# Optimization experiments

Measured on AMD Instinct MI355X. Metric: run time of the kernel, lower is better.

Reference implementation:

```python
import jax, jax.numpy as jnp
import numpy as np

N = 50000        # nodes
E = 800000       # edges (before self-loops)
F_IN = 128       # num_features
HID = 32         # hidden_size per head
HEADS = 4
CLS = 40         # num_classes
NEG_SLOPE = 0.2  # PyG GATConv default leaky_relu slope


def setup_inputs() -> dict:
    key = jax.random.key(0)
    ks = jax.random.split(key, 10)
    s = lambda k, sh: (jax.random.normal(k, sh, jnp.float32) * 0.05)
    x = jax.random.normal(ks[0], (N, F_IN), jnp.float32)
    edge_index = jax.random.randint(ks[1], (2, E), 0, N, dtype=jnp.int64)
    W1 = s(ks[2], (F_IN, HEADS * HID))
    att_src1 = s(ks[3], (HEADS, HID))
    att_dst1 = s(ks[4], (HEADS, HID))
    b1 = jnp.zeros((HEADS * HID,), jnp.float32)
    W2 = s(ks[5], (HEADS * HID, CLS))
    att_src2 = s(ks[6], (1, CLS))
    att_dst2 = s(ks[7], (1, CLS))
    b2 = jnp.zeros((CLS,), jnp.float32)
    return {"x": x, "edge_index": edge_index, "W1": W1, "att_src1": att_src1,
            "att_dst1": att_dst1, "b1": b1, "W2": W2, "att_src2": att_src2,
            "att_dst2": att_dst2, "b2": b2}


def _add_self_loops(edge_index, num_nodes):
    ar = jnp.arange(num_nodes, dtype=edge_index.dtype)
    loops = jnp.stack([ar, ar])
    return jnp.concatenate([edge_index, loops], axis=1)


def _gat_conv(x, edge_index, W, a_src, a_dst, bias, heads, concat):
    """PyG GATConv (eval mode, additive attention, self-loops already added)."""
    n = x.shape[0]
    src, dst = edge_index[0], edge_index[1]
    h = (x @ W).reshape(n, heads, -1)                 # [N, H, C]
    a_s = jnp.einsum('nhc,hc->nh', h, a_src)          # [N, H]
    a_d = jnp.einsum('nhc,hc->nh', h, a_dst)          # [N, H]
    e = jax.nn.leaky_relu(a_s[src] + a_d[dst], NEG_SLOPE)   # [E', H]
    m = jax.ops.segment_max(e, dst, num_segments=n)   # segment softmax over dst
    ex = jnp.exp(e - m[dst])
    den = jax.ops.segment_sum(ex, dst, num_segments=n)
    alpha = ex / den[dst]                             # [E', H]
    out = jax.ops.segment_sum(h[src] * alpha[:, :, None], dst, num_segments=n)
    out = out.reshape(n, -1) if concat else out.mean(axis=1)
    return out + bias


def reference(x, edge_index, W1, att_src1, att_dst1, b1, W2, att_src2, att_dst2, b2):
    ei = _add_self_loops(edge_index, x.shape[0])
    # dropout p=0 in eval -> identity
    h = jax.nn.relu(_gat_conv(x, ei, W1, att_src1, att_dst1, b1, HEADS, True))
    out = _gat_conv(h, ei, W2, att_src2, att_dst2, b2, 1, True)  # heads=1
    return out
```

## Files before the change

### kernel.cpp

```cpp
#include <hip/hip_runtime.h>
#include <cstdint>

#define NODES 50000
#define FIN   128
#define C1    128
#define HEADS 4
#define HID   32
#define CLS   40
#define SLOPE 0.2f

#define NBUCK ((NODES + 255) >> 8)
#define EPB 2048
#define BCAP 8192

__device__ __forceinline__ float lrelu(float v) { return v > 0.f ? v : SLOPE * v; }

__device__ __forceinline__ unsigned short f2bf(float f) {
    union { float f; unsigned u; } v; v.f = f;
    unsigned u = v.u;
    return (unsigned short)((u + 0x7FFFu + ((u >> 16) & 1u)) >> 16);
}
__device__ __forceinline__ float bf2f(unsigned short b) {
    union { unsigned u; float f; } v; v.u = ((unsigned)b) << 16;
    return v.f;
}
__device__ __forceinline__ float bflo(unsigned u) {
    union { unsigned x; float f; } v; v.x = u << 16; return v.f;
}
__device__ __forceinline__ float bfhi(unsigned u) {
    union { unsigned x; float f; } v; v.x = u & 0xffff0000u; return v.f;
}
__device__ __forceinline__ unsigned cvtpk(float a, float b) {
    unsigned r;
    asm("v_cvt_pk_bf16_f32 %0, %1, %2" : "=v"(r) : "v"(a), "v"(b));
    return r;
}

typedef __attribute__((ext_vector_type(8))) short bf16x8;
typedef __attribute__((ext_vector_type(4))) float f32x4;
typedef __attribute__((ext_vector_type(4), aligned(4))) int int4a;

__device__ __forceinline__ void acc8(float w, uint4 p, float* ac) {
    ac[0] = fmaf(w, bflo(p.x), ac[0]); ac[1] = fmaf(w, bfhi(p.x), ac[1]);
    ac[2] = fmaf(w, bflo(p.y), ac[2]); ac[3] = fmaf(w, bfhi(p.y), ac[3]);
    ac[4] = fmaf(w, bflo(p.z), ac[4]); ac[5] = fmaf(w, bfhi(p.z), ac[5]);
    ac[6] = fmaf(w, bflo(p.w), ac[6]); ac[7] = fmaf(w, bfhi(p.w), ac[7]);
}

__global__ __launch_bounds__(256) void k_prep(const float* __restrict__ W1,
                                              const float* __restrict__ W2,
                                              unsigned short* __restrict__ w1t,
                                              unsigned short* __restrict__ w2t,
                                              int* __restrict__ bwp) {
    const int b = blockIdx.x, t = threadIdx.x;
    if (b < 8) {
        __shared__ unsigned short Tb[16][136];
        const int n0 = b * 16;
        const int k = t & 127, g = t >> 7;
#pragma unroll
        for (int i = 0; i < 8; i++)
            Tb[g * 8 + i][k] = f2bf(W1[(size_t)k * C1 + n0 + g * 8 + i]);
        __syncthreads();
        {
            int nl = t >> 4, k8 = (t & 15) * 8;
            *(uint4*)(w1t + (n0 + nl) * 128 + k8) = *(uint4*)(&Tb[nl][k8]);
        }
    } else {
        for (int p = t; p < CLS * 128; p += 256) {
            int n = p >> 7, k = p & 127;
            w2t[n * 128 + k] = f2bf(W2[(size_t)k * CLS + n]);
        }
        if (t < NBUCK) bwp[t] = t * BCAP;
    }
}

__global__ __launch_bounds__(256) void k_front(const float* __restrict__ X,
                                               const unsigned short* __restrict__ w1t,
                                               const float* __restrict__ AS,
                                               const float* __restrict__ AD,
                                               unsigned short* __restrict__ h1b,
                                               float* __restrict__ as1,
                                               float* __restrict__ ad1,
                                               const int* __restrict__ src,
                                               const int* __restrict__ dst, int E,
                                               int* __restrict__ bwp,
                                               int* __restrict__ tmp, int GB1) {
    __shared__ unsigned short Asm[64][136];
    __shared__ unsigned short Wt[128][136];
    __shared__ int cnt[NBUCK];
    __shared__ int bbs[NBUCK];
    const int t = threadIdx.x;

    if (blockIdx.x >= GB1) {
        for (int i = t; i < NBUCK; i += 256) cnt[i] = 0;
        __syncthreads();
        const int e0 = (blockIdx.x - GB1) * EPB;
        int v[8], rb[8];
#pragma unroll
        for (int k = 0; k < 8; k++) {
            int e = e0 + k * 256 + t;
            rb[k] = -1;
            if (e < E) {
                int d = dst[e], s = src[e];
                int b = d >> 8;
                int r = atomicAdd(&cnt[b], 1);
                v[k] = (s << 8) | (d & 255);
                rb[k] = (r << 8) | b;
            }
        }
        __syncthreads();
        for (int i = t; i < NBUCK; i += 256) {
            int c = cnt[i];
            bbs[i] = c ? atomicAdd(&bwp[i], c) : 0;
        }
        __syncthreads();
#pragma unroll
        for (int k = 0; k < 8; k++) {
            if (rb[k] >= 0) {
                int b = rb[k] & 255;
                int r = rb[k] >> 8;
                tmp[bbs[b] + r] = v[k];
            }
        }
        return;
    }

    const int row0 = blockIdx.x * 64;
#pragma unroll
    for (int i = 0; i < 8; i++) {
        int p = i * 256 + t;
        int n = p >> 4, k8 = (p & 15) * 8;
        *(uint4*)(&Wt[n][k8]) = *(const uint4*)(w1t + n * 128 + k8);
    }
    {
        int r = t >> 2, c0 = (t & 3) * 32;
        int gr = row0 + r;
        if (gr < NODES) {
#pragma unroll
            for (int i = 0; i < 4; i++) {
                float4 va = *(const float4*)(X + (size_t)gr * FIN + c0 + i * 8);
                float4 vb = *(const float4*)(X + (size_t)gr * FIN + c0 + i * 8 + 4);
                uint4 pk;
                pk.x = cvtpk(va.x, va.y);
                pk.y = cvtpk(va.z, va.w);
                pk.z = cvtpk(vb.x, vb.y);
                pk.w = cvtpk(vb.z, vb.w);
                *(uint4*)(&Asm[r][c0 + i * 8]) = pk;
            }
        } else {
            uint4 z = make_uint4(0, 0, 0, 0);
#pragma unroll
            for (int i = 0; i < 4; i++) *(uint4*)(&Asm[r][c0 + i * 8]) = z;
        }
    }
    __syncthreads();

    const int w = t >> 6, l = t & 63;
    const int lm = l & 15, quad = l >> 4;
    f32x4 acc[8];
#pragma unroll
    for (int ct = 0; ct < 8; ct++) acc[ct] = (f32x4){0.f, 0.f, 0.f, 0.f};
#pragma unroll
    for (int kt = 0; kt < 4; kt++) {
        bf16x8 a = *(const bf16x8*)(&Asm[w * 16 + lm][kt * 32 + quad * 8]);
#pragma unroll
        for (int ct = 0; ct < 8; ct++) {
            bf16x8 b = *(const bf16x8*)(&Wt[ct * 16 + lm][kt * 32 + quad * 8]);
            acc[ct] = __builtin_amdgcn_mfma_f32_16x16x32_bf16(a, b, acc[ct], 0, 0, 0);
        }
    }
    __syncthreads();
#pragma unroll
    for (int ct = 0; ct < 8; ct++)
#pragma unroll
        for (int r = 0; r < 4; r++)
            Asm[w * 16 + quad * 4 + r][ct * 16 + lm] = f2bf(acc[ct][r]);
    __syncthreads();
    {
        int r = t >> 2, c0 = (t & 3) * 32;
        int gr = row0 + r;
        if (gr < NODES) {
#pragma unroll
            for (int i = 0; i < 4; i++)
                *(uint4*)(h1b + (size_t)gr * C1 + c0 + i * 8) =
                    *(uint4*)(&Asm[r][c0 + i * 8]);
        }
    }
    {
        int r = t >> 2, h = t & 3;
        int gr = row0 + r;
        if (gr < NODES) {
            float s = 0.f, d = 0.f;
#pragma unroll
            for (int j = 0; j < 32; j++) {
                float v = bf2f(Asm[r][h * 32 + j]);
                s = fmaf(v, AS[h * HID + j], s);
                d = fmaf(v, AD[h * HID + j], d);
            }
            as1[gr * HEADS + h] = s;
            ad1[gr * HEADS + h] = d;
        }
    }
}

__global__ __launch_bounds__(256) void k_bucketB(const int* __restrict__ bwp,
                                                 const int* __restrict__ tmp,
                                                 int* __restrict__ col,
                                                 int* __restrict__ rowptr,
                                                 int* __restrict__ degarr) {
    __shared__ int degs[256];
    __shared__ int wp[256];
    __shared__ int wsum[4];
    const int b = blockIdx.x, t = threadIdx.x;
    const int n0 = b << 8;
    const int beg = b * BCAP;
    const int end = bwp[b];
    degs[t] = 0;
    __syncthreads();
    for (int e = beg + t; e < end; e += 256)
        atomicAdd(&degs[tmp[e] & 255], 1);
    __syncthreads();
    const int d = degs[t];
    int incl = d;
    const int lane = t & 63, w = t >> 6;
#pragma unroll
    for (int s = 1; s < 64; s <<= 1) {
        int u = __shfl_up(incl, s);
        if (lane >= s) incl += u;
    }
    if (lane == 63) wsum[w] = incl;
    __syncthreads();
    if (t == 0) {
        int r = 0;
#pragma unroll
        for (int i = 0; i < 4; i++) { int x = wsum[i]; wsum[i] = r; r += x; }
    }
    __syncthreads();
    const int excl = incl - d + wsum[w] + beg;
    const int nidx = n0 + t;
    if (nidx < NODES) { rowptr[nidx] = excl; degarr[nidx] = d; }
    wp[t] = excl;
    __syncthreads();
    for (int e = beg + t; e < end; e += 256) {
        int v = tmp[e];
        int p = atomicAdd(&wp[v & 255], 1);
        col[p] = v >> 8;
    }
}

__global__ __launch_bounds__(256) void k_agg1(const unsigned short* __restrict__ h1b,
                                              const float* __restrict__ as1,
                                              const float* __restrict__ ad1,
                                              const int* __restrict__ rowptr,
                                              const int* __restrict__ degarr,
                                              const int* __restrict__ col,
                                              const float* __restrict__ b1,
                                              unsigned short* __restrict__ out1) {
    int wid = (blockIdx.x * 256 + threadIdx.x) >> 6;
    if (wid >= NODES) return;
    const int lane = threadIdx.x & 63;
    const int q  = lane >> 4;
    const int ll = lane & 15;
    const int fh = ll >> 2;
    const int n = wid;
    const float adn = ad1[n * HEADS + fh];
    const int rs = rowptr[n];
    const int re = rs + degarr[n];

    float den = 0.f;
    float ac[8];
#pragma unroll
    for (int k = 0; k < 8; k++) ac[k] = 0.f;

    for (int base = rs; base < re; base += 32) {
        int4a ca = *(const int4a*)(col + base + q * 4);
        int4a cb = *(const int4a*)(col + base + 16 + q * 4);
        const int ia = base + q * 4;
        const int ib = base + 16 + q * 4;
        int c0 = (ia + 0 < re) ? ca.x : n;
        int c1 = (ia + 1 < re) ? ca.y : n;
        int c2 = (ia + 2 < re) ? ca.z : n;
        int c3 = (ia + 3 < re) ? ca.w : n;
        int c4 = (ib + 0 < re) ? cb.x : n;
        int c5 = (ib + 1 < re) ? cb.y : n;
        int c6 = (ib + 2 < re) ? cb.z : n;
        int c7 = (ib + 3 < re) ? cb.w : n;
        float w0 = __expf(lrelu(as1[c0 * HEADS + fh] + adn)); if (ia + 0 >= re) w0 = 0.f;
        float w1 = __expf(lrelu(as1[c1 * HEADS + fh] + adn)); if (ia + 1 >= re) w1 = 0.f;
        float w2 = __expf(lrelu(as1[c2 * HEADS + fh] + adn)); if (ia + 2 >= re) w2 = 0.f;
        float w3 = __expf(lrelu(as1[c3 * HEADS + fh] + adn)); if (ia + 3 >= re) w3 = 0.f;
        float w4 = __expf(lrelu(as1[c4 * HEADS + fh] + adn)); if (ib + 0 >= re) w4 = 0.f;
        float w5 = __expf(lrelu(as1[c5 * HEADS + fh] + adn)); if (ib + 1 >= re) w5 = 0.f;
        float w6 = __expf(lrelu(as1[c6 * HEADS + fh] + adn)); if (ib + 2 >= re) w6 = 0.f;
        float w7 = __expf(lrelu(as1[c7 * HEADS + fh] + adn)); if (ib + 3 >= re) w7 = 0.f;
        den += ((w0 + w1) + (w2 + w3)) + ((w4 + w5) + (w6 + w7));
        const unsigned lo = (unsigned)(ll << 4);
        uint4 p0 = *(const uint4*)((const char*)h1b + (((unsigned)c0 << 8) + lo));
        uint4 p1 = *(const uint4*)((const char*)h1b + (((unsigned)c1 << 8) + lo));
        uint4 p2 = *(const uint4*)((const char*)h1b + (((unsigned)c2 << 8) + lo));
        uint4 p3 = *(const uint4*)((const char*)h1b + (((unsigned)c3 << 8) + lo));
        uint4 p4 = *(const uint4*)((const char*)h1b + (((unsigned)c4 << 8) + lo));
        uint4 p5 = *(const uint4*)((const char*)h1b + (((unsigned)c5 << 8) + lo));
        uint4 p6 = *(const uint4*)((const char*)h1b + (((unsigned)c6 << 8) + lo));
        uint4 p7 = *(const uint4*)((const char*)h1b + (((unsigned)c7 << 8) + lo));
        acc8(w0, p0, ac); acc8(w1, p1, ac); acc8(w2, p2, ac); acc8(w3, p3, ac);
        acc8(w4, p4, ac); acc8(w5, p5, ac); acc8(w6, p6, ac); acc8(w7, p7, ac);
    }
    den += __shfl_xor(den, 16);
    den += __shfl_xor(den, 32);
#pragma unroll
    for (int k = 0; k < 8; k++) {
        ac[k] += __shfl_xor(ac[k], 16);
        ac[k] += __shfl_xor(ac[k], 32);
    }
    const float wself = __expf(lrelu(as1[n * HEADS + fh] + adn));
    den += wself;
    if (q == 0) {
        unsigned offs = ((unsigned)n << 8) + (unsigned)(ll << 4);
        uint4 sp = *(const uint4*)((const char*)h1b + offs);
        float sv[8] = {bflo(sp.x), bfhi(sp.x), bflo(sp.y), bfhi(sp.y),
                       bflo(sp.z), bfhi(sp.z), bflo(sp.w), bfhi(sp.w)};
        float4 bv0 = *(const float4*)(b1 + ll * 8);
        float4 bv1 = *(const float4*)(b1 + ll * 8 + 4);
        float bb[8] = {bv0.x, bv0.y, bv0.z, bv0.w, bv1.x, bv1.y, bv1.z, bv1.w};
        const float inv = 1.f / den;
        float o[8];
#pragma unroll
        for (int k = 0; k < 8; k++)
            o[k] = fmaxf(fmaf(wself, sv[k], ac[k]) * inv + bb[k], 0.f);
        uint4 pk;
        pk.x = cvtpk(o[0], o[1]);
        pk.y = cvtpk(o[2], o[3]);
        pk.z = cvtpk(o[4], o[5]);
        pk.w = cvtpk(o[6], o[7]);
        *(uint4*)(out1 + (size_t)n * C1 + ll * 8) = pk;
    }
}

__global__ __launch_bounds__(256) void k_gemm2(const unsigned short* __restrict__ out1b,
                                               const unsigned short* __restrict__ w2t,
                                               const float* __restrict__ AS,
                                               const float* __restrict__ AD,
                                               unsigned short* __restrict__ h2b,
                                               float* __restrict__ as2,
                                               float* __restrict__ ad2) {
    __shared__ unsigned short Asm[64][136];
    __shared__ unsigned short Wt2[48][136];
    __shared__ float Cc[64][52];
    const int t = threadIdx.x;
    const int row0 = blockIdx.x * 64;

    for (int p = t; p < 8 * 136; p += 256) Wt2[40 + p / 136][p % 136] = 0;
    for (int p = t; p < 640; p += 256) {
        int n = p >> 4, k8 = (p & 15) * 8;
        *(uint4*)(&Wt2[n][k8]) = *(const uint4*)(w2t + n * 128 + k8);
    }
    {
        int r = t >> 2, c0 = (t & 3) * 32;
        int gr = row0 + r;
        if (gr < NODES) {
#pragma unroll
            for (int i = 0; i < 4; i++)
                *(uint4*)(&Asm[r][c0 + i * 8]) =
                    *(const uint4*)(out1b + (size_t)gr * C1 + c0 + i * 8);
        } else {
            uint4 z = make_uint4(0, 0, 0, 0);
#pragma unroll
            for (int i = 0; i < 4; i++) *(uint4*)(&Asm[r][c0 + i * 8]) = z;
        }
    }
    __syncthreads();

    const int w = t >> 6, l = t & 63;
    const int lm = l & 15, quad = l >> 4;
    f32x4 acc[3];
#pragma unroll
    for (int ct = 0; ct < 3; ct++) acc[ct] = (f32x4){0.f, 0.f, 0.f, 0.f};
#pragma unroll
    for (int kt = 0; kt < 4; kt++) {
        bf16x8 a = *(const bf16x8*)(&Asm[w * 16 + lm][kt * 32 + quad * 8]);
#pragma unroll
        for (int ct = 0; ct < 3; ct++) {
            bf16x8 b = *(const bf16x8*)(&Wt2[ct * 16 + lm][kt * 32 + quad * 8]);
            acc[ct] = __builtin_amdgcn_mfma_f32_16x16x32_bf16(a, b, acc[ct], 0, 0, 0);
        }
    }
    __syncthreads();
#pragma unroll
    for (int ct = 0; ct < 3; ct++)
#pragma unroll
        for (int r = 0; r < 4; r++)
            Cc[w * 16 + quad * 4 + r][ct * 16 + lm] = acc[ct][r];
    __syncthreads();
    {
        int r = t >> 2, c0 = (t & 3) * 10;
        int gr = row0 + r;
        if (gr < NODES) {
#pragma unroll
            for (int i = 0; i < 5; i++) {
                int c = c0 + i * 2;
                unsigned pk = cvtpk(Cc[r][c], Cc[r][c + 1]);
                *(unsigned*)(h2b + (size_t)gr * 64 + c) = pk;
            }
            float s = 0.f, d = 0.f;
#pragma unroll
            for (int j = 0; j < 10; j++) {
                float v = Cc[r][c0 + j];
                s = fmaf(v, AS[c0 + j], s);
                d = fmaf(v, AD[c0 + j], d);
            }
            s += __shfl_xor(s, 1); s += __shfl_xor(s, 2);
            d += __shfl_xor(d, 1); d += __shfl_xor(d, 2);
            if ((t & 3) == 0) { as2[gr] = s; ad2[gr] = d; }
        }
    }
}

__global__ __launch_bounds__(256) void k_agg2(const unsigned short* __restrict__ h2b,
                                              const float* __restrict__ as2,
                                              const float* __restrict__ ad2,
                                              const int* __restrict__ rowptr,
                                              const int* __restrict__ degarr,
                                              const int* __restrict__ col,
                                              const float* __restrict__ b2,
                                              float* __restrict__ out) {
    int wid = (blockIdx.x * 256 + threadIdx.x) >> 6;
    if (wid >= NODES) return;
    const int lane = threadIdx.x & 63;
    const int q8 = lane >> 3, l8 = lane & 7;
    const int n = wid;
    const float adn = ad2[n];
    const int rs = rowptr[n];
    const int re = rs + degarr[n];

    float den = 0.f;
    float ac[8];
#pragma unroll
    for (int k = 0; k < 8; k++) ac[k] = 0.f;

    for (int base = rs; base < re; base += 32) {
        int4a cc = *(const int4a*)(col + base + q8 * 4);
        const int i0 = base + q8 * 4;
        int c0 = (i0 + 0 < re) ? cc.x : n;
        int c1 = (i0 + 1 < re) ? cc.y : n;
        int c2 = (i0 + 2 < re) ? cc.z : n;
        int c3 = (i0 + 3 < re) ? cc.w : n;
        float w0 = __expf(lrelu(as2[c0] + adn)); if (i0 + 0 >= re) w0 = 0.f;
        float w1 = __expf(lrelu(as2[c1] + adn)); if (i0 + 1 >= re) w1 = 0.f;
        float w2 = __expf(lrelu(as2[c2] + adn)); if (i0 + 2 >= re) w2 = 0.f;
        float w3 = __expf(lrelu(as2[c3] + adn)); if (i0 + 3 >= re) w3 = 0.f;
        den += (w0 + w1) + (w2 + w3);
        if (l8 < 5) {
            const unsigned lo = (unsigned)(l8 << 4);
            uint4 p0 = *(const uint4*)((const char*)h2b + (((unsigned)c0 << 7) + lo));
            uint4 p1 = *(const uint4*)((const char*)h2b + (((unsigned)c1 << 7) + lo));
            uint4 p2 = *(const uint4*)((const char*)h2b + (((unsigned)c2 << 7) + lo));
            uint4 p3 = *(const uint4*)((const char*)h2b + (((unsigned)c3 << 7) + lo));
            acc8(w0, p0, ac); acc8(w1, p1, ac);
            acc8(w2, p2, ac); acc8(w3, p3, ac);
        }
    }
    den += __shfl_xor(den, 8);
    den += __shfl_xor(den, 16);
    den += __shfl_xor(den, 32);
#pragma unroll
    for (int k = 0; k < 8; k++) {
        ac[k] += __shfl_xor(ac[k], 8);
        ac[k] += __shfl_xor(ac[k], 16);
        ac[k] += __shfl_xor(ac[k], 32);
    }
    const float wself = __expf(lrelu(as2[n] + adn));
    den += wself;
    if (q8 == 0 && l8 < 5) {
        unsigned offs = ((unsigned)n << 7) + (unsigned)(l8 << 4);
        uint4 sp = *(const uint4*)((const char*)h2b + offs);
        float sv[8] = {bflo(sp.x), bfhi(sp.x), bflo(sp.y), bfhi(sp.y),
                       bflo(sp.z), bfhi(sp.z), bflo(sp.w), bfhi(sp.w)};
        float4 bv0 = *(const float4*)(b2 + l8 * 8);
        float4 bv1 = *(const float4*)(b2 + l8 * 8 + 4);
        float bb[8] = {bv0.x, bv0.y, bv0.z, bv0.w, bv1.x, bv1.y, bv1.z, bv1.w};
        float o[8];
#pragma unroll
        for (int k = 0; k < 8; k++)
            o[k] = (ac[k] + wself * sv[k]) / den + bb[k];
        *(float4*)(out + (size_t)n * CLS + l8 * 8) =
            make_float4(o[0], o[1], o[2], o[3]);
        *(float4*)(out + (size_t)n * CLS + l8 * 8 + 4) =
            make_float4(o[4], o[5], o[6], o[7]);
    }
}

extern "C" void kernel_launch(void* const* d_in, const int* in_sizes, int n_in,
                              void* d_out, int out_size, void* d_ws, size_t ws_size,
                              hipStream_t stream) {
    const float* x     = (const float*)d_in[0];
    const int*   ei    = (const int*)d_in[1];
    const float* W1    = (const float*)d_in[2];
    const float* aS1   = (const float*)d_in[3];
    const float* aD1   = (const float*)d_in[4];
    const float* b1    = (const float*)d_in[5];
    const float* W2    = (const float*)d_in[6];
    const float* aS2   = (const float*)d_in[7];
    const float* aD2   = (const float*)d_in[8];
    const float* b2    = (const float*)d_in[9];
    float* out = (float*)d_out;
    const int E = in_sizes[1] / 2;
    const int* src = ei;
    const int* dst = ei + E;

    char* ws = (char*)d_ws;
    size_t off = 0;
    auto alloc = [&](size_t bytes) -> char* {
        char* p = ws + off;
        off += (bytes + 255) & ~(size_t)255;
        return p;
    };
    unsigned short* h1b  = (unsigned short*)alloc((size_t)NODES * C1 * 2);
    unsigned short* out1 = (unsigned short*)alloc((size_t)NODES * C1 * 2);
    unsigned short* h2b  = (unsigned short*)alloc((size_t)NODES * 64 * 2);
    float* as1    = (float*)alloc((size_t)NODES * HEADS * 4);
    float* ad1    = (float*)alloc((size_t)NODES * HEADS * 4);
    float* as2    = (float*)alloc((size_t)NODES * 4);
    float* ad2    = (float*)alloc((size_t)NODES * 4);
    int* rowptr   = (int*)alloc((size_t)NODES * 4);
    int* degarr   = (int*)alloc((size_t)NODES * 4);
    int* col      = (int*)alloc((size_t)NBUCK * BCAP * 4 + 256);
    int* tmp      = (int*)alloc((size_t)NBUCK * BCAP * 4 + 256);
    unsigned short* w1t = (unsigned short*)alloc((size_t)FIN * C1 * 2);
    unsigned short* w2t = (unsigned short*)alloc((size_t)CLS * 128 * 2);
    int* bwp      = (int*)alloc((size_t)NBUCK * 4);

    const int GB1 = (NODES + 63) / 64;
    const int GBA = (E + EPB - 1) / EPB;

    k_prep<<<9, 256, 0, stream>>>(W1, W2, w1t, w2t, bwp);
    k_front<<<GB1 + GBA, 256, 0, stream>>>(x, w1t, aS1, aD1, h1b, as1, ad1,
                                           src, dst, E, bwp, tmp, GB1);
    k_bucketB<<<NBUCK, 256, 0, stream>>>(bwp, tmp, col, rowptr, degarr);
    k_agg1<<<(NODES * 64) / 256, 256, 0, stream>>>(h1b, as1, ad1, rowptr, degarr,
                                                   col, b1, out1);
    k_gemm2<<<(NODES + 63) / 64, 256, 0, stream>>>(out1, w2t, aS2, aD2, h2b, as2, ad2);
    k_agg2<<<(NODES * 64) / 256, 256, 0, stream>>>(h2b, as2, ad2, rowptr, degarr,
                                                   col, b2, out);
}
```

Before: 207.0 us.

## Process two destination nodes per wave in aggregation and compact h2 layout

Each wavefront in both aggregation kernels now handles two destination nodes with interleaved neighbor loops, to raise memory-level parallelism for the gathers. The h2 buffer row stride drops from 64 to 40 bf16 to cut gather bytes. The bucket-B kernel moves to 512 threads, and the attention-score dot product in the front GEMM uses vectorized LDS reads. Interleaving nodes with unequal degrees wastes lanes while the shorter list idles, and column reads past row ends need padding, which is why the buffers grow.

```diff
diff --git a/kernel.cpp b/kernel.cpp
--- a/kernel.cpp
+++ b/kernel.cpp
@@ -39,6 +39,7 @@
 typedef __attribute__((ext_vector_type(8))) short bf16x8;
 typedef __attribute__((ext_vector_type(4))) float f32x4;
 typedef __attribute__((ext_vector_type(4), aligned(4))) int int4a;
+typedef __attribute__((ext_vector_type(2), aligned(4))) int int2a;
 
 __device__ __forceinline__ void acc8(float w, uint4 p, float* ac) {
     ac[0] = fmaf(w, bflo(p.x), ac[0]); ac[1] = fmaf(w, bfhi(p.x), ac[1]);
@@ -192,10 +193,22 @@
         if (gr < NODES) {
             float s = 0.f, d = 0.f;
 #pragma unroll
-            for (int j = 0; j < 32; j++) {
-                float v = bf2f(Asm[r][h * 32 + j]);
-                s = fmaf(v, AS[h * HID + j], s);
-                d = fmaf(v, AD[h * HID + j], d);
+            for (int i = 0; i < 4; i++) {
+                uint4 hv = *(const uint4*)(&Asm[r][h * 32 + i * 8]);
+                float4 a0 = *(const float4*)(AS + h * HID + i * 8);
+                float4 a1 = *(const float4*)(AS + h * HID + i * 8 + 4);
+                float4 d0 = *(const float4*)(AD + h * HID + i * 8);
+                float4 d1 = *(const float4*)(AD + h * HID + i * 8 + 4);
+                float v0 = bflo(hv.x), v1 = bfhi(hv.x), v2 = bflo(hv.y), v3 = bfhi(hv.y);
+                float v4 = bflo(hv.z), v5 = bfhi(hv.z), v6 = bflo(hv.w), v7 = bfhi(hv.w);
+                s = fmaf(v0, a0.x, s); s = fmaf(v1, a0.y, s);
+                s = fmaf(v2, a0.z, s); s = fmaf(v3, a0.w, s);
+                s = fmaf(v4, a1.x, s); s = fmaf(v5, a1.y, s);
+                s = fmaf(v6, a1.z, s); s = fmaf(v7, a1.w, s);
+                d = fmaf(v0, d0.x, d); d = fmaf(v1, d0.y, d);
+                d = fmaf(v2, d0.z, d); d = fmaf(v3, d0.w, d);
+                d = fmaf(v4, d1.x, d); d = fmaf(v5, d1.y, d);
+                d = fmaf(v6, d1.z, d); d = fmaf(v7, d1.w, d);
             }
             as1[gr * HEADS + h] = s;
             ad1[gr * HEADS + h] = d;
@@ -203,7 +216,7 @@
     }
 }
 
-__global__ __launch_bounds__(256) void k_bucketB(const int* __restrict__ bwp,
+__global__ __launch_bounds__(512) void k_bucketB(const int* __restrict__ bwp,
                                                  const int* __restrict__ tmp,
                                                  int* __restrict__ col,
                                                  int* __restrict__ rowptr,
@@ -215,20 +228,23 @@
     const int n0 = b << 8;
     const int beg = b * BCAP;
     const int end = bwp[b];
-    degs[t] = 0;
-    __syncthreads();
-    for (int e = beg + t; e < end; e += 256)
+    if (t < 256) degs[t] = 0;
+    __syncthreads();
+    for (int e = beg + t; e < end; e += 512)
         atomicAdd(&degs[tmp[e] & 255], 1);
     __syncthreads();
-    const int d = degs[t];
-    int incl = d;
+    int d = 0, incl = 0;
     const int lane = t & 63, w = t >> 6;
-#pragma unroll
-    for (int s = 1; s < 64; s <<= 1) {
-        int u = __shfl_up(incl, s);
-        if (lane >= s) incl += u;
-    }
-    if (lane == 63) wsum[w] = incl;
+    if (t < 256) {
+        d = degs[t];
+        incl = d;
+#pragma unroll
+        for (int s = 1; s < 64; s <<= 1) {
+            int u = __shfl_up(incl, s);
+            if (lane >= s) incl += u;
+        }
+        if (lane == 63) wsum[w] = incl;
+    }
     __syncthreads();
     if (t == 0) {
         int r = 0;
@@ -236,12 +252,14 @@
         for (int i = 0; i < 4; i++) { int x = wsum[i]; wsum[i] = r; r += x; }
     }
     __syncthreads();
-    const int excl = incl - d + wsum[w] + beg;
-    const int nidx = n0 + t;
-    if (nidx < NODES) { rowptr[nidx] = excl; degarr[nidx] = d; }
-    wp[t] = excl;
-    __syncthreads();
-    for (int e = beg + t; e < end; e += 256) {
+    if (t < 256) {
+        const int excl = incl - d + wsum[w] + beg;
+        const int nidx = n0 + t;
+        if (nidx < NODES) { rowptr[nidx] = excl; degarr[nidx] = d; }
+        wp[t] = excl;
+    }
+    __syncthreads();
+    for (int e = beg + t; e < end; e += 512) {
         int v = tmp[e];
         int p = atomicAdd(&wp[v & 255], 1);
         col[p] = v >> 8;
@@ -256,84 +274,103 @@
                                               const int* __restrict__ col,
                                               const float* __restrict__ b1,
                                               unsigned short* __restrict__ out1) {
-    int wid = (blockIdx.x * 256 + threadIdx.x) >> 6;
-    if (wid >= NODES) return;
+    int pid = (blockIdx.x * 256 + threadIdx.x) >> 6;
+    if (pid >= NODES / 2) return;
     const int lane = threadIdx.x & 63;
     const int q  = lane >> 4;
     const int ll = lane & 15;
     const int fh = ll >> 2;
-    const int n = wid;
-    const float adn = ad1[n * HEADS + fh];
-    const int rs = rowptr[n];
-    const int re = rs + degarr[n];
-
-    float den = 0.f;
-    float ac[8];
-#pragma unroll
-    for (int k = 0; k < 8; k++) ac[k] = 0.f;
-
-    for (int base = rs; base < re; base += 32) {
-        int4a ca = *(const int4a*)(col + base + q * 4);
-        int4a cb = *(const int4a*)(col + base + 16 + q * 4);
-        const int ia = base + q * 4;
-        const int ib = base + 16 + q * 4;
-        int c0 = (ia + 0 < re) ? ca.x : n;
-        int c1 = (ia + 1 < re) ? ca.y : n;
-        int c2 = (ia + 2 < re) ? ca.z : n;
-        int c3 = (ia + 3 < re) ? ca.w : n;
-        int c4 = (ib + 0 < re) ? cb.x : n;
-        int c5 = (ib + 1 < re) ? cb.y : n;
-        int c6 = (ib + 2 < re) ? cb.z : n;
-        int c7 = (ib + 3 < re) ? cb.w : n;
-        float w0 = __expf(lrelu(as1[c0 * HEADS + fh] + adn)); if (ia + 0 >= re) w0 = 0.f;
-        float w1 = __expf(lrelu(as1[c1 * HEADS + fh] + adn)); if (ia + 1 >= re) w1 = 0.f;
-        float w2 = __expf(lrelu(as1[c2 * HEADS + fh] + adn)); if (ia + 2 >= re) w2 = 0.f;
-        float w3 = __expf(lrelu(as1[c3 * HEADS + fh] + adn)); if (ia + 3 >= re) w3 = 0.f;
-        float w4 = __expf(lrelu(as1[c4 * HEADS + fh] + adn)); if (ib + 0 >= re) w4 = 0.f;
-        float w5 = __expf(lrelu(as1[c5 * HEADS + fh] + adn)); if (ib + 1 >= re) w5 = 0.f;
-        float w6 = __expf(lrelu(as1[c6 * HEADS + fh] + adn)); if (ib + 2 >= re) w6 = 0.f;
-        float w7 = __expf(lrelu(as1[c7 * HEADS + fh] + adn)); if (ib + 3 >= re) w7 = 0.f;
-        den += ((w0 + w1) + (w2 + w3)) + ((w4 + w5) + (w6 + w7));
-        const unsigned lo = (unsigned)(ll << 4);
-        uint4 p0 = *(const uint4*)((const char*)h1b + (((unsigned)c0 << 8) + lo));
-        uint4 p1 = *(const uint4*)((const char*)h1b + (((unsigned)c1 << 8) + lo));
-        uint4 p2 = *(const uint4*)((const char*)h1b + (((unsigned)c2 << 8) + lo));
-        uint4 p3 = *(const uint4*)((const char*)h1b + (((unsigned)c3 << 8) + lo));
-        uint4 p4 = *(const uint4*)((const char*)h1b + (((unsigned)c4 << 8) + lo));
-        uint4 p5 = *(const uint4*)((const char*)h1b + (((unsigned)c5 << 8) + lo));
-        uint4 p6 = *(const uint4*)((const char*)h1b + (((unsigned)c6 << 8) + lo));
-        uint4 p7 = *(const uint4*)((const char*)h1b + (((unsigned)c7 << 8) + lo));
-        acc8(w0, p0, ac); acc8(w1, p1, ac); acc8(w2, p2, ac); acc8(w3, p3, ac);
-        acc8(w4, p4, ac); acc8(w5, p5, ac); acc8(w6, p6, ac); acc8(w7, p7, ac);
-    }
-    den += __shfl_xor(den, 16);
-    den += __shfl_xor(den, 32);
+    const unsigned lo = (unsigned)(ll << 4);
+    const int nA = pid * 2, nB = nA + 1;
+    const float adA = ad1[nA * HEADS + fh];
+    const float adB = ad1[nB * HEADS + fh];
+    const int rsA = rowptr[nA], reA = rsA + degarr[nA];
+    const int rsB = rowptr[nB], reB = rsB + degarr[nB];
+
+    float denA = 0.f, denB = 0.f;
+    float acA[8], acB[8];
+#pragma unroll
+    for (int k = 0; k < 8; k++) { acA[k] = 0.f; acB[k] = 0.f; }
+
+    int baseA = rsA, baseB = rsB;
+    while (baseA < reA || baseB < reB) {
+        int4a cA = *(const int4a*)(col + baseA + q * 4);
+        int4a cB = *(const int4a*)(col + baseB + q * 4);
+        const int iA = baseA + q * 4, iB = baseB + q * 4;
+        int a0 = (iA + 0 < reA) ? cA.x : nA;
+        int a1 = (iA + 1 < reA) ? cA.y : nA;
+        int a2 = (iA + 2 < reA) ? cA.z : nA;
+        int a3 = (iA + 3 < reA) ? cA.w : nA;
+        int b0 = (iB + 0 < reB) ? cB.x : nB;
+        int b1i = (iB + 1 < reB) ? cB.y : nB;
+        int b2 = (iB + 2 < reB) ? cB.z : nB;
+        int b3 = (iB + 3 < reB) ? cB.w : nB;
+        float wa0 = __expf(lrelu(as1[a0 * HEADS + fh] + adA)); if (iA + 0 >= reA) wa0 = 0.f;
+        float wa1 = __expf(lrelu(as1[a1 * HEADS + fh] + adA)); if (iA + 1 >= reA) wa1 = 0.f;
+        float wa2 = __expf(lrelu(as1[a2 * HEADS + fh] + adA)); if (iA + 2 >= reA) wa2 = 0.f;
+        float wa3 = __expf(lrelu(as1[a3 * HEADS + fh] + adA)); if (iA + 3 >= reA) wa3 = 0.f;
+        float wb0 = __expf(lrelu(as1[b0 * HEADS + fh] + adB)); if (iB + 0 >= reB) wb0 = 0.f;
+        float wb1 = __expf(lrelu(as1[b1i * HEADS + fh] + adB)); if (iB + 1 >= reB) wb1 = 0.f;
+        float wb2 = __expf(lrelu(as1[b2 * HEADS + fh] + adB)); if (iB + 2 >= reB) wb2 = 0.f;
+        float wb3 = __expf(lrelu(as1[b3 * HEADS + fh] + adB)); if (iB + 3 >= reB) wb3 = 0.f;
+        denA += (wa0 + wa1) + (wa2 + wa3);
+        denB += (wb0 + wb1) + (wb2 + wb3);
+        uint4 pa0 = *(const uint4*)((const char*)h1b + (((unsigned)a0 << 8) + lo));
+        uint4 pa1 = *(const uint4*)((const char*)h1b + (((unsigned)a1 << 8) + lo));
+        uint4 pa2 = *(const uint4*)((const char*)h1b + (((unsigned)a2 << 8) + lo));
+        uint4 pa3 = *(const uint4*)((const char*)h1b + (((unsigned)a3 << 8) + lo));
+        uint4 pb0 = *(const uint4*)((const char*)h1b + (((unsigned)b0 << 8) + lo));
+        uint4 pb1 = *(const uint4*)((const char*)h1b + (((unsigned)b1i << 8) + lo));
+        uint4 pb2 = *(const uint4*)((const char*)h1b + (((unsigned)b2 << 8) + lo));
+        uint4 pb3 = *(const uint4*)((const char*)h1b + (((unsigned)b3 << 8) + lo));
+        acc8(wa0, pa0, acA); acc8(wa1, pa1, acA);
+        acc8(wa2, pa2, acA); acc8(wa3, pa3, acA);
+        acc8(wb0, pb0, acB); acc8(wb1, pb1, acB);
+        acc8(wb2, pb2, acB); acc8(wb3, pb3, acB);
+        baseA += 16; baseB += 16;
+    }
+    denA += __shfl_xor(denA, 16); denA += __shfl_xor(denA, 32);
+    denB += __shfl_xor(denB, 16); denB += __shfl_xor(denB, 32);
 #pragma unroll
     for (int k = 0; k < 8; k++) {
-        ac[k] += __shfl_xor(ac[k], 16);
-        ac[k] += __shfl_xor(ac[k], 32);
-    }
-    const float wself = __expf(lrelu(as1[n * HEADS + fh] + adn));
-    den += wself;
+        acA[k] += __shfl_xor(acA[k], 16); acA[k] += __shfl_xor(acA[k], 32);
+        acB[k] += __shfl_xor(acB[k], 16); acB[k] += __shfl_xor(acB[k], 32);
+    }
+    const float wsA = __expf(lrelu(as1[nA * HEADS + fh] + adA));
+    const float wsB = __expf(lrelu(as1[nB * HEADS + fh] + adB));
+    denA += wsA; denB += wsB;
     if (q == 0) {
-        unsigned offs = ((unsigned)n << 8) + (unsigned)(ll << 4);
-        uint4 sp = *(const uint4*)((const char*)h1b + offs);
-        float sv[8] = {bflo(sp.x), bfhi(sp.x), bflo(sp.y), bfhi(sp.y),
-                       bflo(sp.z), bfhi(sp.z), bflo(sp.w), bfhi(sp.w)};
         float4 bv0 = *(const float4*)(b1 + ll * 8);
         float4 bv1 = *(const float4*)(b1 + ll * 8 + 4);
         float bb[8] = {bv0.x, bv0.y, bv0.z, bv0.w, bv1.x, bv1.y, bv1.z, bv1.w};
-        const float inv = 1.f / den;
-        float o[8];
-#pragma unroll
-        for (int k = 0; k < 8; k++)
-            o[k] = fmaxf(fmaf(wself, sv[k], ac[k]) * inv + bb[k], 0.f);
-        uint4 pk;
-        pk.x = cvtpk(o[0], o[1]);
-        pk.y = cvtpk(o[2], o[3]);
-        pk.z = cvtpk(o[4], o[5]);
-        pk.w = cvtpk(o[6], o[7]);
-        *(uint4*)(out1 + (size_t)n * C1 + ll * 8) = pk;
+        {
+            uint4 sp = *(const uint4*)((const char*)h1b + (((unsigned)nA << 8) + lo));
+            float sv[8] = {bflo(sp.x), bfhi(sp.x), bflo(sp.y), bfhi(sp.y),
+                           bflo(sp.z), bfhi(sp.z), bflo(sp.w), bfhi(sp.w)};
+            const float inv = 1.f / denA;
+            float o[8];
+#pragma unroll
+            for (int k = 0; k < 8; k++)
+                o[k] = fmaxf(fmaf(wsA, sv[k], acA[k]) * inv + bb[k], 0.f);
+            uint4 pk;
+            pk.x = cvtpk(o[0], o[1]); pk.y = cvtpk(o[2], o[3]);
+            pk.z = cvtpk(o[4], o[5]); pk.w = cvtpk(o[6], o[7]);
+            *(uint4*)(out1 + (size_t)nA * C1 + ll * 8) = pk;
+        }
+        {
+            uint4 sp = *(const uint4*)((const char*)h1b + (((unsigned)nB << 8) + lo));
+            float sv[8] = {bflo(sp.x), bfhi(sp.x), bflo(sp.y), bfhi(sp.y),
+                           bflo(sp.z), bfhi(sp.z), bflo(sp.w), bfhi(sp.w)};
+            const float inv = 1.f / denB;
+            float o[8];
+#pragma unroll
+            for (int k = 0; k < 8; k++)
+                o[k] = fmaxf(fmaf(wsB, sv[k], acB[k]) * inv + bb[k], 0.f);
+            uint4 pk;
+            pk.x = cvtpk(o[0], o[1]); pk.y = cvtpk(o[2], o[3]);
+            pk.z = cvtpk(o[4], o[5]); pk.w = cvtpk(o[6], o[7]);
+            *(uint4*)(out1 + (size_t)nB * C1 + ll * 8) = pk;
+        }
     }
 }
 
@@ -400,7 +437,7 @@
             for (int i = 0; i < 5; i++) {
                 int c = c0 + i * 2;
                 unsigned pk = cvtpk(Cc[r][c], Cc[r][c + 1]);
-                *(unsigned*)(h2b + (size_t)gr * 64 + c) = pk;
+                *(unsigned*)(h2b + (size_t)gr * 40 + c) = pk;
             }
             float s = 0.f, d = 0.f;
 #pragma unroll
@@ -424,69 +461,88 @@
                                               const int* __restrict__ col,
                                               const float* __restrict__ b2,
                                               float* __restrict__ out) {
-    int wid = (blockIdx.x * 256 + threadIdx.x) >> 6;
-    if (wid >= NODES) return;
+    int pid = (blockIdx.x * 256 + threadIdx.x) >> 6;
+    if (pid >= NODES / 2) return;
     const int lane = threadIdx.x & 63;
     const int q8 = lane >> 3, l8 = lane & 7;
-    const int n = wid;
-    const float adn = ad2[n];
-    const int rs = rowptr[n];
-    const int re = rs + degarr[n];
-
-    float den = 0.f;
-    float ac[8];
-#pragma unroll
-    for (int k = 0; k < 8; k++) ac[k] = 0.f;
-
-    for (int base = rs; base < re; base += 32) {
-        int4a cc = *(const int4a*)(col + base + q8 * 4);
-        const int i0 = base + q8 * 4;
-        int c0 = (i0 + 0 < re) ? cc.x : n;
-        int c1 = (i0 + 1 < re) ? cc.y : n;
-        int c2 = (i0 + 2 < re) ? cc.z : n;
-        int c3 = (i0 + 3 < re) ? cc.w : n;
-        float w0 = __expf(lrelu(as2[c0] + adn)); if (i0 + 0 >= re) w0 = 0.f;
-        float w1 = __expf(lrelu(as2[c1] + adn)); if (i0 + 1 >= re) w1 = 0.f;
-        float w2 = __expf(lrelu(as2[c2] + adn)); if (i0 + 2 >= re) w2 = 0.f;
-        float w3 = __expf(lrelu(as2[c3] + adn)); if (i0 + 3 >= re) w3 = 0.f;
-        den += (w0 + w1) + (w2 + w3);
+    const unsigned lo = (unsigned)(l8 << 4);
+    const int nA = pid * 2, nB = nA + 1;
+    const float adA = ad2[nA], adB = ad2[nB];
+    const int rsA = rowptr[nA], reA = rsA + degarr[nA];
+    const int rsB = rowptr[nB], reB = rsB + degarr[nB];
+
+    float denA = 0.f, denB = 0.f;
+    float acA[8], acB[8];
+#pragma unroll
+    for (int k = 0; k < 8; k++) { acA[k] = 0.f; acB[k] = 0.f; }
+
+    int baseA = rsA, baseB = rsB;
+    while (baseA < reA || baseB < reB) {
+        int2a cA = *(const int2a*)(col + baseA + q8 * 2);
+        int2a cB = *(const int2a*)(col + baseB + q8 * 2);
+        const int iA = baseA + q8 * 2, iB = baseB + q8 * 2;
+        int a0 = (iA + 0 < reA) ? cA.x : nA;
+        int a1 = (iA + 1 < reA) ? cA.y : nA;
+        int b0 = (iB + 0 < reB) ? cB.x : nB;
+        int b1i = (iB + 1 < reB) ? cB.y : nB;
+        float wa0 = __expf(lrelu(as2[a0] + adA)); if (iA + 0 >= reA) wa0 = 0.f;
+        float wa1 = __expf(lrelu(as2[a1] + adA)); if (iA + 1 >= reA) wa1 = 0.f;
+        float wb0 = __expf(lrelu(as2[b0] + adB)); if (iB + 0 >= reB) wb0 = 0.f;
+        float wb1 = __expf(lrelu(as2[b1i] + adB)); if (iB + 1 >= reB) wb1 = 0.f;
+        denA += wa0 + wa1;
+        denB += wb0 + wb1;
         if (l8 < 5) {
-            const unsigned lo = (unsigned)(l8 << 4);
-            uint4 p0 = *(const uint4*)((const char*)h2b + (((unsigned)c0 << 7) + lo));
-            uint4 p1 = *(const uint4*)((const char*)h2b + (((unsigned)c1 << 7) + lo));
-            uint4 p2 = *(const uint4*)((const char*)h2b + (((unsigned)c2 << 7) + lo));
-            uint4 p3 = *(const uint4*)((const char*)h2b + (((unsigned)c3 << 7) + lo));
-            acc8(w0, p0, ac); acc8(w1, p1, ac);
-            acc8(w2, p2, ac); acc8(w3, p3, ac);
-        }
-    }
-    den += __shfl_xor(den, 8);
-    den += __shfl_xor(den, 16);
-    den += __shfl_xor(den, 32);
+            uint4 pa0 = *(const uint4*)((const char*)h2b + ((unsigned)a0 * 80u + lo));
+            uint4 pa1 = *(const uint4*)((const char*)h2b + ((unsigned)a1 * 80u + lo));
+            uint4 pb0 = *(const uint4*)((const char*)h2b + ((unsigned)b0 * 80u + lo));
+            uint4 pb1 = *(const uint4*)((const char*)h2b + ((unsigned)b1i * 80u + lo));
+            acc8(wa0, pa0, acA); acc8(wa1, pa1, acA);
+            acc8(wb0, pb0, acB); acc8(wb1, pb1, acB);
+        }
+        baseA += 16; baseB += 16;
+    }
+    denA += __shfl_xor(denA, 8); denA += __shfl_xor(denA, 16); denA += __shfl_xor(denA, 32);
+    denB += __shfl_xor(denB, 8); denB += __shfl_xor(denB, 16); denB += __shfl_xor(denB, 32);
 #pragma unroll
     for (int k = 0; k < 8; k++) {
-        ac[k] += __shfl_xor(ac[k], 8);
-        ac[k] += __shfl_xor(ac[k], 16);
-        ac[k] += __shfl_xor(ac[k], 32);
-    }
-    const float wself = __expf(lrelu(as2[n] + adn));
-    den += wself;
+        acA[k] += __shfl_xor(acA[k], 8); acA[k] += __shfl_xor(acA[k], 16);
+        acA[k] += __shfl_xor(acA[k], 32);
+        acB[k] += __shfl_xor(acB[k], 8); acB[k] += __shfl_xor(acB[k], 16);
+        acB[k] += __shfl_xor(acB[k], 32);
+    }
+    const float wsA = __expf(lrelu(as2[nA] + adA));
+    const float wsB = __expf(lrelu(as2[nB] + adB));
+    denA += wsA; denB += wsB;
     if (q8 == 0 && l8 < 5) {
-        unsigned offs = ((unsigned)n << 7) + (unsigned)(l8 << 4);
-        uint4 sp = *(const uint4*)((const char*)h2b + offs);
-        float sv[8] = {bflo(sp.x), bfhi(sp.x), bflo(sp.y), bfhi(sp.y),
-                       bflo(sp.z), bfhi(sp.z), bflo(sp.w), bfhi(sp.w)};
         float4 bv0 = *(const float4*)(b2 + l8 * 8);
         float4 bv1 = *(const float4*)(b2 + l8 * 8 + 4);
         float bb[8] = {bv0.x, bv0.y, bv0.z, bv0.w, bv1.x, bv1.y, bv1.z, bv1.w};
-        float o[8];
-#pragma unroll
-        for (int k = 0; k < 8; k++)
-            o[k] = (ac[k] + wself * sv[k]) / den + bb[k];
-        *(float4*)(out + (size_t)n * CLS + l8 * 8) =
-            make_float4(o[0], o[1], o[2], o[3]);
-        *(float4*)(out + (size_t)n * CLS + l8 * 8 + 4) =
-            make_float4(o[4], o[5], o[6], o[7]);
+        {
+            uint4 sp = *(const uint4*)((const char*)h2b + ((unsigned)nA * 80u + lo));
+            float sv[8] = {bflo(sp.x), bfhi(sp.x), bflo(sp.y), bfhi(sp.y),
+                           bflo(sp.z), bfhi(sp.z), bflo(sp.w), bfhi(sp.w)};
+            float o[8];
+#pragma unroll
+            for (int k = 0; k < 8; k++)
+                o[k] = (acA[k] + wsA * sv[k]) / denA + bb[k];
+            *(float4*)(out + (size_t)nA * CLS + l8 * 8) =
+                make_float4(o[0], o[1], o[2], o[3]);
+            *(float4*)(out + (size_t)nA * CLS + l8 * 8 + 4) =
+                make_float4(o[4], o[5], o[6], o[7]);
+        }
+        {
+            uint4 sp = *(const uint4*)((const char*)h2b + ((unsigned)nB * 80u + lo));
+            float sv[8] = {bflo(sp.x), bfhi(sp.x), bflo(sp.y), bfhi(sp.y),
+                           bflo(sp.z), bfhi(sp.z), bflo(sp.w), bfhi(sp.w)};
+            float o[8];
+#pragma unroll
+            for (int k = 0; k < 8; k++)
+                o[k] = (acB[k] + wsB * sv[k]) / denB + bb[k];
+            *(float4*)(out + (size_t)nB * CLS + l8 * 8) =
+                make_float4(o[0], o[1], o[2], o[3]);
+            *(float4*)(out + (size_t)nB * CLS + l8 * 8 + 4) =
+                make_float4(o[4], o[5], o[6], o[7]);
+        }
     }
 }
 
@@ -517,15 +573,15 @@
     };
     unsigned short* h1b  = (unsigned short*)alloc((size_t)NODES * C1 * 2);
     unsigned short* out1 = (unsigned short*)alloc((size_t)NODES * C1 * 2);
-    unsigned short* h2b  = (unsigned short*)alloc((size_t)NODES * 64 * 2);
+    unsigned short* h2b  = (unsigned short*)alloc((size_t)NODES * 40 * 2);
     float* as1    = (float*)alloc((size_t)NODES * HEADS * 4);
     float* ad1    = (float*)alloc((size_t)NODES * HEADS * 4);
     float* as2    = (float*)alloc((size_t)NODES * 4);
     float* ad2    = (float*)alloc((size_t)NODES * 4);
     int* rowptr   = (int*)alloc((size_t)NODES * 4);
     int* degarr   = (int*)alloc((size_t)NODES * 4);
-    int* col      = (int*)alloc((size_t)NBUCK * BCAP * 4 + 256);
-    int* tmp      = (int*)alloc((size_t)NBUCK * BCAP * 4 + 256);
+    int* col      = (int*)alloc((size_t)NBUCK * BCAP * 4 + 1024);
+    int* tmp      = (int*)alloc((size_t)NBUCK * BCAP * 4 + 1024);
     unsigned short* w1t = (unsigned short*)alloc((size_t)FIN * C1 * 2);
     unsigned short* w2t = (unsigned short*)alloc((size_t)CLS * 128 * 2);
     int* bwp      = (int*)alloc((size_t)NBUCK * 4);
@@ -536,10 +592,10 @@
     k_prep<<<9, 256, 0, stream>>>(W1, W2, w1t, w2t, bwp);
     k_front<<<GB1 + GBA, 256, 0, stream>>>(x, w1t, aS1, aD1, h1b, as1, ad1,
                                            src, dst, E, bwp, tmp, GB1);
-    k_bucketB<<<NBUCK, 256, 0, stream>>>(bwp, tmp, col, rowptr, degarr);
-    k_agg1<<<(NODES * 64) / 256, 256, 0, stream>>>(h1b, as1, ad1, rowptr, degarr,
-                                                   col, b1, out1);
+    k_bucketB<<<NBUCK, 512, 0, stream>>>(bwp, tmp, col, rowptr, degarr);
+    k_agg1<<<(NODES / 2 * 64) / 256, 256, 0, stream>>>(h1b, as1, ad1, rowptr, degarr,
+                                                       col, b1, out1);
     k_gemm2<<<(NODES + 63) / 64, 256, 0, stream>>>(out1, w2t, aS2, aD2, h2b, as2, ad2);
-    k_agg2<<<(NODES * 64) / 256, 256, 0, stream>>>(h2b, as2, ad2, rowptr, degarr,
-                                                   col, b2, out);
-}
+    k_agg2<<<(NODES / 2 * 64) / 256, 256, 0, stream>>>(h2b, as2, ad2, rowptr, degarr,
+                                                       col, b2, out);
+}
```

Measured after the change: 194.7 us. 5.9% less time.
